# Optimization experiments

Measured on AMD Instinct MI355X. Metric: run time of the kernel, lower is better.

## Reference

```python
import jax, jax.numpy as jnp
import numpy as np

SIGMA_MIN, SIGMA_MAX = 0.03, 0.35
LAMBDA_GEO = 8.0
COMPAT_SCALE = 0.1
INVALID_W = 0.05
NH, HD = 8, 64
LN_EPS = 1e-5

def _ln(x, g, b):
    m = x.mean(-1, keepdims=True)
    v = ((x - m) ** 2).mean(-1, keepdims=True)
    return (x - m) * jax.lax.rsqrt(v + LN_EPS) * g + b

def setup_inputs() -> dict:
    key = jax.random.key(0)
    ks = jax.random.split(key, 32)
    B, C, H, W = 8, 512, 32, 32
    T, S, D, SIN = 1024, 1024, 512, 512
    s = 0.02
    inp = {
        'front_feat': jax.random.normal(ks[0], (B, C, H, W), jnp.float32),
        'sat_tokens': jax.random.normal(ks[1], (B, S, SIN), jnp.float32),
        'sat_xy': jax.random.uniform(ks[2], (B, S, 2), jnp.float32),
        'front_bev_xy': jax.random.uniform(ks[3], (B, T, 2), jnp.float32),
        'front_bev_valid_mask': jax.random.bernoulli(ks[4], 0.9, (B, T)),
        'front_plucker': jax.random.normal(ks[5], (B, T, 6), jnp.float32),
        'fa_w': jax.random.normal(ks[6], (C, D), jnp.float32) * s,
        'fa_b': jnp.zeros((D,), jnp.float32),
        'fa_g': jnp.ones((D,), jnp.float32),
        'fa_lb': jnp.zeros((D,), jnp.float32),
        'sa_w': jax.random.normal(ks[7], (SIN, D), jnp.float32) * s,
        'sa_b': jnp.zeros((D,), jnp.float32),
        'sa_g': jnp.ones((D,), jnp.float32),
        'sa_lb': jnp.zeros((D,), jnp.float32),
        'q_w': jax.random.normal(ks[8], (D, D), jnp.float32) * s,
        'q_b': jnp.zeros((D,), jnp.float32),
        'k_w': jax.random.normal(ks[9], (D, D), jnp.float32) * s,
        'k_b': jnp.zeros((D,), jnp.float32),
        'v_w': jax.random.normal(ks[10], (D, D), jnp.float32) * s,
        'v_b': jnp.zeros((D,), jnp.float32),
        'pl_w1': jax.random.normal(ks[11], (6, D), jnp.float32) * s,
        'pl_b1': jnp.zeros((D,), jnp.float32),
        'pl_w2': jax.random.normal(ks[12], (D, D), jnp.float32) * s,
        'pl_b2': jnp.zeros((D,), jnp.float32),
        'sig_w': jax.random.normal(ks[13], (D, 1), jnp.float32) * s,
        'sig_b': jnp.zeros((1,), jnp.float32),
        'db_w': jax.random.normal(ks[14], (D, NH), jnp.float32) * s,
        'db_b': jnp.zeros((NH,), jnp.float32),
        'out_w': jax.random.normal(ks[15], (D, C), jnp.float32) * s,
        'out_b': jnp.zeros((C,), jnp.float32),
    }
    return inp

def _forward(front_feat, sat_tokens, sat_xy, front_bev_xy, front_plucker,
             fa_w, fa_b, fa_g, fa_lb, sa_w, sa_b, sa_g, sa_lb,
             q_w, q_b, k_w, k_b, v_w, v_b, pl_w1, pl_b1, pl_w2, pl_b2,
             sig_w, sig_b, db_w, db_b, out_w, out_b, valid_mask):
    B, C, H, W = front_feat.shape
    T = H * W
    D = NH * HD
    front_flat = front_feat.reshape(B, C, T).transpose(0, 2, 1)  # [B,T,C]
    front_embed = _ln(front_flat @ fa_w + fa_b, fa_g, fa_lb)
    pl = jax.nn.silu(front_plucker @ pl_w1 + pl_b1) @ pl_w2 + pl_b2
    context = front_embed + pl
    sat_embed = _ln(sat_tokens @ sa_w + sa_b, sa_g, sa_lb)
    def heads(x):
        return x.reshape(B, -1, NH, HD).transpose(0, 2, 1, 3)  # [B,H,N,d]
    q = heads(front_embed @ q_w + q_b)
    k = heads(sat_embed @ k_w + k_b)
    v = heads(sat_embed @ v_w + v_b)
    compat = jnp.einsum('bhtd,bhsd->bhts', q, k) / jnp.sqrt(jnp.float32(HD))
    compat = COMPAT_SCALE * compat
    sigma = SIGMA_MIN + (SIGMA_MAX - SIGMA_MIN) * jax.nn.sigmoid((context @ sig_w + sig_b)[..., 0])  # [B,T]
    dist2 = ((front_bev_xy[:, :, None, :] - sat_xy[:, None, :, :]) ** 2).sum(-1)  # [B,T,S]
    geo = -LAMBDA_GEO * dist2 / jnp.maximum(sigma[..., None] ** 2, 1e-6)
    sat_logits = compat + geo[:, None]  # [B,H,T,S]
    sat_logits = jnp.where(valid_mask[:, None, :, None], sat_logits, jnp.float32(-10000.0))
    dustbin = (context @ db_w + db_b).transpose(0, 2, 1)[..., None]  # [B,H,T,1]
    logits = jnp.concatenate([sat_logits, dustbin], axis=-1)
    probs = jax.nn.softmax(logits, axis=-1)
    sat_probs, dustbin_prob = probs[..., :-1], probs[..., -1]
    read = jnp.einsum('bhts,bhsd->bhtd', sat_probs, v)
    read = read.transpose(0, 2, 1, 3).reshape(B, T, D)
    read_feat = (read @ out_w + out_b).transpose(0, 2, 1).reshape(B, C, H, W)
    confidence = (1.0 - dustbin_prob).mean(axis=1)  # [B,T]
    conf_feat = confidence.reshape(B, 1, H, W)
    front_feat_out = front_feat + conf_feat * read_feat
    vf = valid_mask.astype(confidence.dtype)
    inv = 1.0 - vf
    invalid_conf = (confidence * inv).sum() / jnp.maximum(inv.sum(), 1.0)
    invalid_conf_loss = invalid_conf * INVALID_W
    return front_feat_out, read_feat, confidence, invalid_conf_loss

def reference(front_feat, sat_tokens, sat_xy, front_bev_xy, front_bev_valid_mask, front_plucker,
              fa_w, fa_b, fa_g, fa_lb, sa_w, sa_b, sa_g, sa_lb,
              q_w, q_b, k_w, k_b, v_w, v_b, pl_w1, pl_b1, pl_w2, pl_b2,
              sig_w, sig_b, db_w, db_b, out_w, out_b):
    return _forward(front_feat, sat_tokens, sat_xy, front_bev_xy, front_plucker,
                    fa_w, fa_b, fa_g, fa_lb, sa_w, sa_b, sa_g, sa_lb,
                    q_w, q_b, k_w, k_b, v_w, v_b, pl_w1, pl_b1, pl_w2, pl_b2,
                    sig_w, sig_b, db_w, db_b, out_w, out_b, front_bev_valid_mask)
```

## Files before the change

kernel.cpp:

```cpp
#include <hip/hip_runtime.h>

typedef unsigned short u16;
typedef __attribute__((ext_vector_type(8))) short short8;
typedef __attribute__((ext_vector_type(4))) float f32x4;

constexpr int B_  = 8;
constexpr int C_  = 512;
constexpr int T_  = 1024;
constexpr int S_  = 1024;
constexpr int D_  = 512;
constexpr int NH_ = 8;
constexpr int BT_ = B_ * T_;
constexpr float INVLN2 = 1.44269504088896340736f;
constexpr float QSCALE2 = 0.0125f * INVLN2;

__device__ __forceinline__ unsigned pack2(float lo, float hi) {
    unsigned r;
    asm("v_cvt_pk_bf16_f32 %0, %1, %2" : "=v"(r) : "v"(lo), "v"(hi));
    return r;
}
__device__ __forceinline__ u16 f2bf(float x) {
    return (u16)pack2(x, x);
}
__device__ __forceinline__ float bf2f(u16 h) {
    union { unsigned u; float f; } v; v.u = ((unsigned)h) << 16;
    return v.f;
}
__device__ __forceinline__ float fexp2(float x) {
    float r;
    asm("v_exp_f32 %0, %1" : "=v"(r) : "v"(x));
    return r;
}
__device__ __forceinline__ float max3f(float a, float b, float c) {
    float r;
    asm("v_max3_f32 %0, %1, %2, %3" : "=v"(r) : "v"(a), "v"(b), "v"(c));
    return r;
}

#define GWAITBAR(N) do { \
    asm volatile("s_waitcnt vmcnt(" #N ") lgkmcnt(0)" ::: "memory"); \
    __builtin_amdgcn_sched_barrier(0); \
    __builtin_amdgcn_s_barrier(); \
    __builtin_amdgcn_sched_barrier(0); } while (0)

typedef __attribute__((address_space(3))) unsigned int lds_u32;
typedef const __attribute__((address_space(1))) unsigned int glob_u32;
__device__ __forceinline__ void g2l16(void* l, const void* g) {
    __builtin_amdgcn_global_load_lds((glob_u32*)g, (lds_u32*)l, 16, 0, 0);
}

__device__ __forceinline__ int is_valid(const void* mask, int mode, int idx) {
    if (mode == 0) return ((const int*)mask)[idx] != 0;
    if (mode == 1) return ((const float*)mask)[idx] != 0.0f;
    return ((const unsigned char*)mask)[idx] != 0;
}

__global__ __launch_bounds__(256) void prep_k(
    const float* __restrict__ ff, const float* __restrict__ sat,
    const float* __restrict__ pl,
    const float* a0, const float* a1, const float* a2, const float* a3,
    const float* a4, const float* a5, u16* __restrict__ WT,
    u16* __restrict__ ffb, u16* __restrict__ satb,
    const float* __restrict__ plw1, const float* __restrict__ plb1,
    u16* __restrict__ plh,
    const unsigned* __restrict__ maskw, int* __restrict__ mode,
    float* __restrict__ scal,
    const float* __restrict__ plw2, const float* __restrict__ sigw,
    const float* __restrict__ dbw, const float* __restrict__ plb2,
    float* __restrict__ wsig, float* __restrict__ wdbf,
    float* __restrict__ offs) {
    __shared__ float tile[32][33];
    int blk = blockIdx.x, tid = threadIdx.x;
    if (blk < 4096) {
        int t0 = (blk & 31) * 32, c0 = ((blk >> 5) & 15) * 32, b = blk >> 9;
        int tx = tid & 31, ty = tid >> 5;
        const float* ip = ff + (size_t)b * C_ * T_;
        for (int i = ty; i < 32; i += 8)
            tile[i][tx] = ip[(size_t)(c0 + i) * T_ + t0 + tx];
        __syncthreads();
        u16* op = ffb + (size_t)b * T_ * C_;
        for (int i = ty; i < 32; i += 8)
            op[(size_t)(t0 + i) * C_ + c0 + tx] = f2bf(tile[tx][i]);
    } else if (blk < 5632) {
        int idx = blk - 4096;
        const float* srcs[6] = {a0, a1, a2, a3, a4, a5};
        int z = idx >> 8;
        const float* src = srcs[z];
        u16* d = WT + (size_t)z * 512 * 512;
        int k0 = (idx & 15) * 32, n0 = ((idx >> 4) & 15) * 32;
        int tx = tid & 31, ty = tid >> 5;
        for (int i = ty; i < 32; i += 8)
            tile[i][tx] = src[(size_t)(k0 + i) * 512 + n0 + tx];
        __syncthreads();
        for (int i = ty; i < 32; i += 8)
            d[(size_t)(n0 + i) * 512 + k0 + tx] = f2bf(tile[tx][i]);
    } else if (blk < 7680) {
        int i = (blk - 5632) * 256 + tid;
        const float4* p = (const float4*)(sat + (size_t)i * 8);
        float4 a = p[0], b = p[1];
        uint4 o;
        o.x = pack2(a.x, a.y); o.y = pack2(a.z, a.w);
        o.z = pack2(b.x, b.y); o.w = pack2(b.z, b.w);
        *(uint4*)(satb + (size_t)i * 8) = o;
    } else if (blk < 9728) {
        int m = (blk - 7680) * 4 + (tid >> 6);
        int lane = tid & 63;
        float p6[6];
#pragma unroll
        for (int j = 0; j < 6; ++j) p6[j] = pl[(size_t)m * 6 + j];
        int n0 = lane * 8;
        float acc[8];
#pragma unroll
        for (int e = 0; e < 8; ++e) acc[e] = plb1[n0 + e];
#pragma unroll
        for (int j = 0; j < 6; ++j) {
            float4 wv0 = *(const float4*)(plw1 + j * D_ + n0);
            float4 wv1 = *(const float4*)(plw1 + j * D_ + n0 + 4);
            acc[0] += p6[j] * wv0.x; acc[1] += p6[j] * wv0.y;
            acc[2] += p6[j] * wv0.z; acc[3] += p6[j] * wv0.w;
            acc[4] += p6[j] * wv1.x; acc[5] += p6[j] * wv1.y;
            acc[6] += p6[j] * wv1.z; acc[7] += p6[j] * wv1.w;
        }
        uint4 o;
        float s0 = acc[0] / (1.0f + __expf(-acc[0]));
        float s1 = acc[1] / (1.0f + __expf(-acc[1]));
        float s2 = acc[2] / (1.0f + __expf(-acc[2]));
        float s3 = acc[3] / (1.0f + __expf(-acc[3]));
        float s4 = acc[4] / (1.0f + __expf(-acc[4]));
        float s5 = acc[5] / (1.0f + __expf(-acc[5]));
        float s6 = acc[6] / (1.0f + __expf(-acc[6]));
        float s7 = acc[7] / (1.0f + __expf(-acc[7]));
        o.x = pack2(s0, s1); o.y = pack2(s2, s3);
        o.z = pack2(s4, s5); o.w = pack2(s6, s7);
        *(uint4*)(plh + (size_t)m * D_ + n0) = o;
    } else if (blk == 9728) {
        __shared__ int bad_i, bad_f;
        if (tid == 0) { bad_i = 0; bad_f = 0; }
        __syncthreads();
        for (int i = tid; i < 2048; i += 256) {
            unsigned v = maskw[i];
            if (v > 1u) bad_i = 1;
            if (v != 0u && v != 0x3f800000u) bad_f = 1;
        }
        __syncthreads();
        if (tid == 0) {
            *mode = (!bad_i) ? 0 : ((!bad_f) ? 1 : 2);
            scal[0] = 0.0f; scal[1] = 0.0f;
        }
    } else if (blk < 9731) {
        int k = (blk - 9729) * 256 + tid;
        const float* wr = plw2 + (size_t)k * 512;
        float acc = 0;
        for (int n = 0; n < 512; n += 4) {
            float4 wv = *(const float4*)(wr + n);
            float4 sv = *(const float4*)(sigw + n);
            acc += wv.x * sv.x + wv.y * sv.y + wv.z * sv.z + wv.w * sv.w;
        }
        wsig[k] = acc;
    } else if (blk < 9747) {
        int idx = blk - 9731;
        int k = idx * 32 + (tid >> 3), h = tid & 7;
        const float* wr = plw2 + (size_t)k * 512;
        float acc = 0;
        for (int n = 0; n < 512; ++n) acc += wr[n] * dbw[n * 8 + h];
        wdbf[k * 8 + h] = acc;
    } else {
        float p = plb2[tid] * sigw[tid] + plb2[tid + 256] * sigw[tid + 256];
        float ph[8];
#pragma unroll
        for (int h = 0; h < 8; ++h)
            ph[h] = plb2[tid] * dbw[tid * 8 + h] +
                    plb2[tid + 256] * dbw[(tid + 256) * 8 + h];
        for (int o = 32; o; o >>= 1) {
            p += __shfl_down(p, o);
#pragma unroll
            for (int h = 0; h < 8; ++h) ph[h] += __shfl_down(ph[h], o);
        }
        __shared__ float red[4][9];
        int wv = tid >> 6, lane = tid & 63;
        if (lane == 0) {
            red[wv][0] = p;
#pragma unroll
            for (int h = 0; h < 8; ++h) red[wv][1 + h] = ph[h];
        }
        __syncthreads();
        if (tid == 0) {
            for (int j = 0; j < 9; ++j) {
                float t = 0;
                for (int v2 = 0; v2 < 4; ++v2) t += red[v2][j];
                offs[j] = t;
            }
        }
    }
}

__global__ __launch_bounds__(256) void gmm_k(
    const u16* __restrict__ A0, const u16* __restrict__ A1,
    const u16* __restrict__ A2, const u16* __restrict__ A3,
    const u16* __restrict__ Bt0, const u16* __restrict__ Bt1,
    const u16* __restrict__ Bt2, const u16* __restrict__ Bt3,
    const float* __restrict__ bb0, const float* __restrict__ bb1,
    const float* __restrict__ bb2, const float* __restrict__ bb3,
    void* __restrict__ C0v, void* __restrict__ C1v,
    void* __restrict__ C2v, void* __restrict__ C3v,
    int md0, int md1, int md2, int md3,
    const u16* __restrict__ addend,
    const float* __restrict__ ffp, float* __restrict__ out1p,
    const float* __restrict__ dbpp, const void* __restrict__ maskp,
    const int* __restrict__ modep, float* __restrict__ outcp,
    float* __restrict__ scalp) {
    __shared__ u16 As[3][4096];
    __shared__ u16 Bs[3][4096];
    __shared__ float confL[128];
    int jid = blockIdx.x >> 8;
    int L = blockIdx.x & 255;
    const u16* A    = (jid == 0) ? A0 : (jid == 1) ? A1 : (jid == 2) ? A2 : A3;
    const u16* Bt   = (jid == 0) ? Bt0 : (jid == 1) ? Bt1 : (jid == 2) ? Bt2 : Bt3;
    const float* bias = (jid == 0) ? bb0 : (jid == 1) ? bb1 : (jid == 2) ? bb2 : bb3;
    void* Cv        = (jid == 0) ? C0v : (jid == 1) ? C1v : (jid == 2) ? C2v : C3v;
    int mode        = (jid == 0) ? md0 : (jid == 1) ? md1 : (jid == 2) ? md2 : md3;

    int tid = threadIdx.x, w = tid >> 6, l = tid & 63;
    int lr = l & 15, g = l >> 4;
    int W = (L & 7) * 32 + (L >> 3);
    int m0 = (W >> 2) * 128, n0 = (W & 3) * 128;
    int wr = w >> 1, wc = w & 1;
    int prm = g ^ ((lr >> 1) & 3);

    f32x4 acc[4][4] = {};

    if (mode == 4 && tid < 128) {
        int row = m0 + tid;
        const float* dr = dbpp + (size_t)row * NH_;
        float s = 0;
#pragma unroll
        for (int h = 0; h < 8; ++h) s += dr[h];
        float cf = 1.0f - s * 0.125f;
        confL[tid] = cf;
        if ((W & 3) == 0) {
            outcp[row] = cf;
            int md = *modep;
            float invd = is_valid(maskp, md, row) ? 0.0f : 1.0f;
            float a = cf * invd, bsum = invd;
            for (int o = 32; o; o >>= 1) {
                a += __shfl_down(a, o);
                bsum += __shfl_down(bsum, o);
            }
            if ((tid & 63) == 0) {
                atomicAdd(&scalp[0], a);
                atomicAdd(&scalp[1], bsum);
            }
        }
    }

    auto stage = [&](int buf, int k0) {
#pragma unroll
        for (int j = 0; j < 2; ++j) {
            int i = tid + 256 * j;
            int row = i >> 2, gg = (i & 3) ^ ((i >> 3) & 3);
            g2l16((char*)As[buf] + (size_t)i * 16,
                  A + (size_t)(m0 + row) * 512 + k0 + gg * 8);
        }
#pragma unroll
        for (int j = 0; j < 2; ++j) {
            int i = tid + 256 * j;
            int col = i >> 2, gg = (i & 3) ^ ((i >> 3) & 3);
            g2l16((char*)Bs[buf] + (size_t)i * 16,
                  Bt + (size_t)(n0 + col) * 512 + k0 + gg * 8);
        }
    };

    auto compute = [&](int bi) {
        const char* Ab = (const char*)As[bi];
        const char* Bb = (const char*)Bs[bi];
        short8 af[4], bf[4];
#pragma unroll
        for (int m = 0; m < 4; ++m)
            af[m] = *(const short8*)(Ab + ((wr * 64 + m * 16 + lr) * 4 + prm) * 16);
#pragma unroll
        for (int n = 0; n < 4; ++n)
            bf[n] = *(const short8*)(Bb + ((wc * 64 + n * 16 + lr) * 4 + prm) * 16);
        __builtin_amdgcn_s_setprio(1);
#pragma unroll
        for (int m = 0; m < 4; ++m)
#pragma unroll
            for (int n = 0; n < 4; ++n)
                acc[m][n] = __builtin_amdgcn_mfma_f32_16x16x32_bf16(
                    af[m], bf[n], acc[m][n], 0, 0, 0);
        __builtin_amdgcn_s_setprio(0);
    };

    stage(0, 0);
    stage(1, 32);
    for (int t = 0; t < 14; ++t) {
        stage((t + 2) % 3, (t + 2) * 32);
        GWAITBAR(8);
        compute(t % 3);
        __builtin_amdgcn_s_barrier();
    }
    GWAITBAR(4);
    compute(2);
    GWAITBAR(0);
    compute(0);

    float bs[4];
#pragma unroll
    for (int n = 0; n < 4; ++n) bs[n] = bias[n0 + wc * 64 + n * 16 + lr];

#pragma unroll
    for (int m = 0; m < 4; ++m) {
#pragma unroll
        for (int n = 0; n < 4; ++n) {
            int R0  = m0 + wr * 64 + m * 16 + 4 * g;
            int col = n0 + wc * 64 + n * 16 + lr;
            if (mode == 3) {
                int bbx = R0 >> 10, ss = R0 & 1023, hh = col >> 6, dd = col & 63;
                uint2 pk;
                pk.x = pack2(acc[m][n][0] + bs[n], acc[m][n][1] + bs[n]);
                pk.y = pack2(acc[m][n][2] + bs[n], acc[m][n][3] + bs[n]);
                u16* dst = (u16*)Cv + ((size_t)(bbx * 8 + hh) * 64 + dd) * 1024 + ss;
                *(uint2*)dst = pk;
            } else if (mode == 4) {
                int bbx = R0 >> 10, t0p = R0 & 1023;
                size_t base = (size_t)bbx * C_ * T_ + (size_t)col * T_ + t0p;
                float4 rf;
                rf.x = acc[m][n][0] + bs[n]; rf.y = acc[m][n][1] + bs[n];
                rf.z = acc[m][n][2] + bs[n]; rf.w = acc[m][n][3] + bs[n];
                float4 ffv = *(const float4*)(ffp + base);
                float4 cfv = *(const float4*)&confL[R0 - m0];
                float4 o0v;
                o0v.x = ffv.x + cfv.x * rf.x; o0v.y = ffv.y + cfv.y * rf.y;
                o0v.z = ffv.z + cfv.z * rf.z; o0v.w = ffv.w + cfv.w * rf.w;
                *(float4*)(out1p + base) = rf;
                *(float4*)((float*)Cv + base) = o0v;
            } else {
#pragma unroll
                for (int j = 0; j < 4; ++j) {
                    int row = R0 + j;
                    float v = acc[m][n][j] + bs[n];
                    if (mode == 1) v *= QSCALE2;
                    if (mode == 2) v += bf2f(addend[(size_t)row * 512 + col]);
                    ((u16*)Cv)[(size_t)row * 512 + col] = f2bf(v);
                }
            }
        }
    }
}

__global__ __launch_bounds__(256) void lnh_k(
    const u16* __restrict__ Epre, const float* __restrict__ fg,
    const float* __restrict__ fb, u16* __restrict__ Eout,
    const u16* __restrict__ Spre, const float* __restrict__ sg,
    const float* __restrict__ sb, u16* __restrict__ Sout,
    const u16* __restrict__ PLH,
    const float* __restrict__ sigw, const float* __restrict__ sigb,
    const float* __restrict__ dbw, const float* __restrict__ dbb,
    const float* __restrict__ wsig, const float* __restrict__ wdbf,
    const float* __restrict__ offs,
    float* __restrict__ sigma, float* __restrict__ dbo) {
    int blk = blockIdx.x, tid = threadIdx.x;
    int wv = tid >> 6, lane = tid & 63;
    if (blk < 4096) {
        int sel = blk >> 11;
        int row = (blk & 2047) * 4 + wv;
        const u16* X = sel ? Spre : Epre;
        const float* gw = sel ? sg : fg;
        const float* bw = sel ? sb : fb;
        u16* out = sel ? Sout : Eout;
        uint4 u = *((const uint4*)(X + (size_t)row * 512) + lane);
        float x[8];
        x[0] = bf2f((u16)(u.x & 0xffff)); x[1] = bf2f((u16)(u.x >> 16));
        x[2] = bf2f((u16)(u.y & 0xffff)); x[3] = bf2f((u16)(u.y >> 16));
        x[4] = bf2f((u16)(u.z & 0xffff)); x[5] = bf2f((u16)(u.z >> 16));
        x[6] = bf2f((u16)(u.w & 0xffff)); x[7] = bf2f((u16)(u.w >> 16));
        float s = 0, sq = 0;
#pragma unroll
        for (int i = 0; i < 8; ++i) { s += x[i]; sq += x[i] * x[i]; }
        for (int o = 1; o < 64; o <<= 1) {
            s += __shfl_xor(s, o); sq += __shfl_xor(sq, o);
        }
        float mean = s * (1.0f / D_);
        float var  = sq * (1.0f / D_) - mean * mean;
        float r = rsqrtf(var + 1e-5f);
        float4 g0v = *(const float4*)(gw + lane * 8);
        float4 g1v = *(const float4*)(gw + lane * 8 + 4);
        float4 b0v = *(const float4*)(bw + lane * 8);
        float4 b1v = *(const float4*)(bw + lane * 8 + 4);
        float gv[8] = {g0v.x, g0v.y, g0v.z, g0v.w, g1v.x, g1v.y, g1v.z, g1v.w};
        float bv[8] = {b0v.x, b0v.y, b0v.z, b0v.w, b1v.x, b1v.y, b1v.z, b1v.w};
        uint4 o;
        float y[8];
#pragma unroll
        for (int i = 0; i < 8; ++i) y[i] = (x[i] - mean) * r * gv[i] + bv[i];
        o.x = pack2(y[0], y[1]); o.y = pack2(y[2], y[3]);
        o.z = pack2(y[4], y[5]); o.w = pack2(y[6], y[7]);
        *((uint4*)(out + (size_t)row * 512) + lane) = o;
    } else {
        int row = (blk - 4096) * 4 + wv;
        uint4 u = *((const uint4*)(Epre + (size_t)row * 512) + lane);
        float x[8];
        x[0] = bf2f((u16)(u.x & 0xffff)); x[1] = bf2f((u16)(u.x >> 16));
        x[2] = bf2f((u16)(u.y & 0xffff)); x[3] = bf2f((u16)(u.y >> 16));
        x[4] = bf2f((u16)(u.z & 0xffff)); x[5] = bf2f((u16)(u.z >> 16));
        x[6] = bf2f((u16)(u.w & 0xffff)); x[7] = bf2f((u16)(u.w >> 16));
        float s = 0, sq = 0;
#pragma unroll
        for (int i = 0; i < 8; ++i) { s += x[i]; sq += x[i] * x[i]; }
        for (int o = 1; o < 64; o <<= 1) {
            s += __shfl_xor(s, o); sq += __shfl_xor(sq, o);
        }
        float mean = s * (1.0f / D_);
        float var  = sq * (1.0f / D_) - mean * mean;
        float r = rsqrtf(var + 1e-5f);
        float4 g0v = *(const float4*)(fg + lane * 8);
        float4 g1v = *(const float4*)(fg + lane * 8 + 4);
        float4 b0v = *(const float4*)(fb + lane * 8);
        float4 b1v = *(const float4*)(fb + lane * 8 + 4);
        float gv[8] = {g0v.x, g0v.y, g0v.z, g0v.w, g1v.x, g1v.y, g1v.z, g1v.w};
        float bv[8] = {b0v.x, b0v.y, b0v.z, b0v.w, b1v.x, b1v.y, b1v.z, b1v.w};
        float E[8];
#pragma unroll
        for (int i = 0; i < 8; ++i) E[i] = (x[i] - mean) * r * gv[i] + bv[i];
        uint4 up = *((const uint4*)(PLH + (size_t)row * 512) + lane);
        float plv[8];
        plv[0] = bf2f((u16)(up.x & 0xffff)); plv[1] = bf2f((u16)(up.x >> 16));
        plv[2] = bf2f((u16)(up.y & 0xffff)); plv[3] = bf2f((u16)(up.y >> 16));
        plv[4] = bf2f((u16)(up.z & 0xffff)); plv[5] = bf2f((u16)(up.z >> 16));
        plv[6] = bf2f((u16)(up.w & 0xffff)); plv[7] = bf2f((u16)(up.w >> 16));
        float4 sw0 = *(const float4*)(sigw + lane * 8);
        float4 sw1 = *(const float4*)(sigw + lane * 8 + 4);
        float4 fw0 = *(const float4*)(wsig + lane * 8);
        float4 fw1 = *(const float4*)(wsig + lane * 8 + 4);
        float swv[8] = {sw0.x, sw0.y, sw0.z, sw0.w, sw1.x, sw1.y, sw1.z, sw1.w};
        float fwv[8] = {fw0.x, fw0.y, fw0.z, fw0.w, fw1.x, fw1.y, fw1.z, fw1.w};
        float sacc = 0;
#pragma unroll
        for (int i = 0; i < 8; ++i) sacc += E[i] * swv[i] + plv[i] * fwv[i];
        float d_[8] = {};
        const float* dr = dbw + (size_t)lane * 8 * NH_;
        const float* fr = wdbf + (size_t)lane * 8 * NH_;
#pragma unroll
        for (int i = 0; i < 8; ++i) {
#pragma unroll
            for (int h = 0; h < 8; ++h)
                d_[h] += E[i] * dr[i * NH_ + h] + plv[i] * fr[i * NH_ + h];
        }
        for (int o = 1; o < 64; o <<= 1) {
            sacc += __shfl_xor(sacc, o);
#pragma unroll
            for (int h = 0; h < 8; ++h) d_[h] += __shfl_xor(d_[h], o);
        }
        if (lane == 0) {
            float z = sacc + sigb[0] + offs[0];
            sigma[row] = 0.03f + 0.32f / (1.0f + __expf(-z));
            float* dd = dbo + (size_t)row * NH_;
#pragma unroll
            for (int h = 0; h < 8; ++h) dd[h] = d_[h] + dbb[h] + offs[1 + h];
        }
    }
}

__global__ __launch_bounds__(512) void attn_k(
    const u16* __restrict__ Q, const u16* __restrict__ K,
    const u16* __restrict__ Vt, const float* __restrict__ sig,
    const float* __restrict__ dbl, const float* __restrict__ bev,
    const float* __restrict__ sxy, const void* __restrict__ mask,
    const int* __restrict__ mode, u16* __restrict__ OUT,
    float* __restrict__ dbp) {
    int L = blockIdx.x;
    int W = (L & 7) * 64 + (L >> 3);
    int b = W >> 6, h = (W >> 3) & 7, tblk = W & 7;
    int tid = threadIdx.x, w = tid >> 6, l = tid & 63;
    int lr = l & 15, g = l >> 4;
    int p8 = lr & 7;

    __shared__ u16 Kbuf[2][4096];
    __shared__ u16 Vbuf[2][4096];
    __shared__ float2 SXY[1024];
    __shared__ float  SZ[1024];

    const float2* xp = (const float2*)(sxy + (size_t)b * S_ * 2);
#pragma unroll
    for (int j = 0; j < 2; ++j) {
        int idx = tid + 512 * j;
        float2 v = xp[idx];
        SXY[idx] = make_float2(-2.0f * v.x, -2.0f * v.y);
        SZ[idx] = v.x * v.x + v.y * v.y;
    }

    int trow = b * T_ + tblk * 128 + w * 16 + lr;
    float s_ = sig[trow];
    float bx = bev[(size_t)trow * 2], by = bev[(size_t)trow * 2 + 1];
    float dbv2 = dbl[(size_t)trow * NH_ + h] * INVLN2;
    int md = *mode;
    bool vld = is_valid(mask, md, trow) != 0;
    float grow  = vld ? (-11.5415603271117f / fmaxf(s_ * s_, 1e-6f)) : 0.0f;
    float Abase = vld ? grow * (bx * bx + by * by) : -10000.0f;
    float AbaseM = Abase - dbv2;
    float mshift = 0.0f;

    const u16* qp = Q + (size_t)trow * 512 + h * 64 + g * 8;
    short8 q0 = *(const short8*)qp;
    short8 q1 = *(const short8*)(qp + 32);
    if (!vld) { q0 = short8{}; q1 = short8{}; }

    short8 ones;
#pragma unroll
    for (int e = 0; e < 8; ++e) ones[e] = (short)0x3F80;

    const u16* Kp = K + (size_t)b * S_ * 512 + h * 64;
    const u16* Vp = Vt + (size_t)(b * 8 + h) * 64 * 1024;

    int srow = tid >> 3;
    int gprm = (tid & 7) ^ (srow & 7);
    int sK = ((srow >> 5) & 1) * 32 + ((srow >> 2) & 3) * 8 +
             ((srow >> 4) & 1) * 4 + (srow & 3);

    auto stageKV = [&](int buf, int s0) {
        g2l16((char*)Kbuf[buf] + (size_t)tid * 16,
              Kp + (size_t)(s0 + sK) * 512 + gprm * 8);
        g2l16((char*)Vbuf[buf] + (size_t)tid * 16,
              Vp + (size_t)srow * 1024 + s0 + gprm * 8);
    };

    f32x4 o0 = {}, o1 = {}, o2 = {}, o3 = {};
    f32x4 o4 = {1.0f, 1.0f, 1.0f, 1.0f};

    stageKV(0, 0);
    int cur = 0;
    for (int c = 0; c < 16; ++c) {
        int s0c = c * 64;
        if (c < 15) {
            stageKV(cur ^ 1, s0c + 64);
            GWAITBAR(2);
        } else {
            GWAITBAR(0);
        }

        const char* Kc = (const char*)Kbuf[cur];
        const char* Vc = (const char*)Vbuf[cur];

        f32x4 p[4];
        f32x4 z4 = {};
        __builtin_amdgcn_s_setprio(1);
#pragma unroll
        for (int sub = 0; sub < 4; ++sub) {
            int krow = sub * 16 + lr;
            short8 kf0 = *(const short8*)(Kc + (krow * 8 + (g ^ p8)) * 16);
            short8 kf1 = *(const short8*)(Kc + (krow * 8 + ((4 + g) ^ p8)) * 16);
            p[sub] = __builtin_amdgcn_mfma_f32_16x16x32_bf16(kf0, q0, z4, 0, 0, 0);
            p[sub] = __builtin_amdgcn_mfma_f32_16x16x32_bf16(kf1, q1, p[sub], 0, 0, 0);
        }
        __builtin_amdgcn_s_setprio(0);

        float lg[16];
#pragma unroll
        for (int sub = 0; sub < 4; ++sub) {
            int sl = s0c + ((sub & 2) << 4) + 8 * g + ((sub & 1) << 2);
            float4 xy01 = *(const float4*)&SXY[sl];
            float4 xy23 = *(const float4*)&SXY[sl + 2];
            float4 zz   = *(const float4*)&SZ[sl];
            float X[4] = {xy01.x, xy01.z, xy23.x, xy23.z};
            float Y[4] = {xy01.y, xy01.w, xy23.y, xy23.w};
            float Z[4] = {zz.x, zz.y, zz.z, zz.w};
#pragma unroll
            for (int i2 = 0; i2 < 4; ++i2) {
                float wg = fmaf(bx, X[i2], fmaf(by, Y[i2], Z[i2]));
                lg[sub * 4 + i2] = fmaf(grow, wg, p[sub][i2] + AbaseM);
            }
        }
        float c0 = max3f(lg[0], lg[1], lg[2]);
        float c1 = max3f(lg[3], lg[4], lg[5]);
        float c2 = max3f(lg[6], lg[7], lg[8]);
        float c3 = max3f(lg[9], lg[10], lg[11]);
        float c4 = max3f(lg[12], lg[13], lg[14]);
        float cl = fmaxf(max3f(c0, c1, c2), max3f(c3, c4, lg[15]));

        if (!__all(cl <= 11.5f)) {
            cl = fmaxf(cl, __shfl_xor(cl, 16));
            cl = fmaxf(cl, __shfl_xor(cl, 32));
            float dm = fmaxf(cl, 0.0f);
            float scl = fexp2(-dm);
            o0 *= scl; o1 *= scl; o2 *= scl; o3 *= scl; o4 *= scl;
            AbaseM -= dm;
            mshift -= dm;
#pragma unroll
            for (int r = 0; r < 16; ++r) lg[r] -= dm;
        }
        float pe[16];
#pragma unroll
        for (int r = 0; r < 16; ++r) pe[r] = fexp2(lg[r]);

        union { uint4 u; short8 s8; } pf0, pf1;
        pf0.u.x = pack2(pe[0], pe[1]);  pf0.u.y = pack2(pe[2], pe[3]);
        pf0.u.z = pack2(pe[4], pe[5]);  pf0.u.w = pack2(pe[6], pe[7]);
        pf1.u.x = pack2(pe[8], pe[9]);  pf1.u.y = pack2(pe[10], pe[11]);
        pf1.u.z = pack2(pe[12], pe[13]); pf1.u.w = pack2(pe[14], pe[15]);

        __builtin_amdgcn_s_setprio(1);
        short8 vf;
#pragma unroll
        for (int dt = 0; dt < 4; ++dt) {
            int vrow = dt * 16 + lr;
            f32x4* oo = (dt == 0) ? &o0 : (dt == 1) ? &o1 : (dt == 2) ? &o2 : &o3;
            vf = *(const short8*)(Vc + (vrow * 8 + (g ^ p8)) * 16);
            *oo = __builtin_amdgcn_mfma_f32_16x16x32_bf16(vf, pf0.s8, *oo, 0, 0, 0);
            vf = *(const short8*)(Vc + (vrow * 8 + ((4 + g) ^ p8)) * 16);
            *oo = __builtin_amdgcn_mfma_f32_16x16x32_bf16(vf, pf1.s8, *oo, 0, 0, 0);
        }
        o4 = __builtin_amdgcn_mfma_f32_16x16x32_bf16(ones, pf0.s8, o4, 0, 0, 0);
        o4 = __builtin_amdgcn_mfma_f32_16x16x32_bf16(ones, pf1.s8, o4, 0, 0, 0);
        __builtin_amdgcn_s_setprio(0);

        __builtin_amdgcn_s_barrier();
        cur ^= 1;
    }

    float inv = 1.0f / o4[0];
    u16* ob = OUT + (size_t)trow * 512 + h * 64;
    {
        uint2 pk;
        pk.x = pack2(o0[0] * inv, o0[1] * inv); pk.y = pack2(o0[2] * inv, o0[3] * inv);
        *(uint2*)(ob + 0 * 16 + 4 * g) = pk;
        pk.x = pack2(o1[0] * inv, o1[1] * inv); pk.y = pack2(o1[2] * inv, o1[3] * inv);
        *(uint2*)(ob + 1 * 16 + 4 * g) = pk;
        pk.x = pack2(o2[0] * inv, o2[1] * inv); pk.y = pack2(o2[2] * inv, o2[3] * inv);
        *(uint2*)(ob + 2 * 16 + 4 * g) = pk;
        pk.x = pack2(o3[0] * inv, o3[1] * inv); pk.y = pack2(o3[2] * inv, o3[3] * inv);
        *(uint2*)(ob + 3 * 16 + 4 * g) = pk;
    }
    if (g == 0) dbp[(size_t)trow * NH_ + h] = fexp2(mshift) * inv;
}

__global__ void loss_k(const float* __restrict__ scal, float* __restrict__ out) {
    out[0] = scal[0] / fmaxf(scal[1], 1.0f) * 0.05f;
}

extern "C" void kernel_launch(void* const* d_in, const int* in_sizes, int n_in,
                              void* d_out, int out_size, void* d_ws, size_t ws_size,
                              hipStream_t stream) {
    const float* front_feat = (const float*)d_in[0];
    const float* sat_tokens = (const float*)d_in[1];
    const float* sat_xy     = (const float*)d_in[2];
    const float* bev_xy     = (const float*)d_in[3];
    const void*  mask       = d_in[4];
    const float* plucker    = (const float*)d_in[5];
    const float* fa_w = (const float*)d_in[6];
    const float* fa_b = (const float*)d_in[7];
    const float* fa_g = (const float*)d_in[8];
    const float* fa_lb = (const float*)d_in[9];
    const float* sa_w = (const float*)d_in[10];
    const float* sa_b = (const float*)d_in[11];
    const float* sa_g = (const float*)d_in[12];
    const float* sa_lb = (const float*)d_in[13];
    const float* q_w = (const float*)d_in[14];
    const float* q_b = (const float*)d_in[15];
    const float* k_w = (const float*)d_in[16];
    const float* k_b = (const float*)d_in[17];
    const float* v_w = (const float*)d_in[18];
    const float* v_b = (const float*)d_in[19];
    const float* pl_w1 = (const float*)d_in[20];
    const float* pl_b1 = (const float*)d_in[21];
    const float* pl_w2 = (const float*)d_in[22];
    const float* pl_b2 = (const float*)d_in[23];
    const float* sig_w = (const float*)d_in[24];
    const float* sig_b = (const float*)d_in[25];
    const float* db_w = (const float*)d_in[26];
    const float* db_b = (const float*)d_in[27];
    const float* out_w = (const float*)d_in[28];
    const float* out_b = (const float*)d_in[29];

    char* w8 = (char*)d_ws;
    u16* H0 = (u16*)(w8);
    u16* H1 = (u16*)(w8 + 8388608ull * 1);
    u16* H2 = (u16*)(w8 + 8388608ull * 2);
    u16* H3 = (u16*)(w8 + 8388608ull * 3);
    u16* H4 = (u16*)(w8 + 8388608ull * 4);
    u16* H5 = (u16*)(w8 + 8388608ull * 5);
    u16* H6 = (u16*)(w8 + 8388608ull * 6);
    u16* WT = (u16*)(w8 + 8388608ull * 7);
    char* sm = w8 + 8388608ull * 7 + 3670016ull;
    float* w_sigma = (float*)sm;
    float* w_db    = w_sigma + BT_;
    float* w_dbp   = w_db + (size_t)BT_ * NH_;
    float* w_scal  = w_dbp + (size_t)BT_ * NH_;
    int*   w_mode  = (int*)(w_scal + 2);
    float* w_wsig  = w_scal + 4;
    float* w_wdbf  = w_wsig + 512;
    float* w_offs  = w_wdbf + 4096;

    u16* Wfa = WT;                 u16* Wq  = WT + 262144ull * 1;
    u16* Wsa = WT + 262144ull * 2; u16* Wk  = WT + 262144ull * 3;
    u16* Wv  = WT + 262144ull * 4; u16* Wo  = WT + 262144ull * 5;

    float* out0 = (float*)d_out;
    float* out1 = out0 + (size_t)B_ * C_ * T_;
    float* outc = out1 + (size_t)B_ * C_ * T_;
    float* outl = outc + (size_t)B_ * T_;

    dim3 blk(256);

    prep_k<<<dim3(9748), blk, 0, stream>>>(
        front_feat, sat_tokens, plucker,
        fa_w, q_w, sa_w, k_w, v_w, out_w, WT,
        H0, H5, pl_w1, pl_b1, H2,
        (const unsigned*)mask, w_mode, w_scal,
        pl_w2, sig_w, db_w, pl_b2, w_wsig, w_wdbf, w_offs);
    gmm_k<<<dim3(512), blk, 0, stream>>>(
        H0, H5, nullptr, nullptr,
        Wfa, Wsa, nullptr, nullptr,
        fa_b, sa_b, nullptr, nullptr,
        H6, H4, nullptr, nullptr,
        0, 0, 0, 0,
        nullptr, nullptr, nullptr,
        nullptr, nullptr, nullptr, nullptr, nullptr);
    lnh_k<<<dim3(6144), blk, 0, stream>>>(
        H6, fa_g, fa_lb, H1,
        H4, sa_g, sa_lb, H3,
        H2, sig_w, sig_b, db_w, db_b,
        w_wsig, w_wdbf, w_offs, w_sigma, w_db);
    gmm_k<<<dim3(768), blk, 0, stream>>>(
        H1, H3, H3, nullptr,
        Wq, Wk, Wv, nullptr,
        q_b, k_b, v_b, nullptr,
        H5, H0, H4, nullptr,
        1, 0, 3, 0,
        nullptr, nullptr, nullptr,
        nullptr, nullptr, nullptr, nullptr, nullptr);
    attn_k<<<dim3(512), dim3(512), 0, stream>>>(
        H5, H0, H4, w_sigma, w_db, bev_xy, sat_xy, mask, w_mode, H2, w_dbp);
    gmm_k<<<dim3(256), blk, 0, stream>>>(
        H2, nullptr, nullptr, nullptr,
        Wo, nullptr, nullptr, nullptr,
        out_b, nullptr, nullptr, nullptr,
        out0, nullptr, nullptr, nullptr,
        4, 0, 0, 0,
        nullptr, front_feat, out1,
        w_dbp, mask, w_mode, outc, w_scal);
    loss_k<<<1, 1, 0, stream>>>(w_scal, outl);
}
```

Measured before the change: 170.3 us.

## Split LayerNorm and head projection kernels, transpose dustbin weights for vector loads

```diff
diff --git a/kernel.cpp b/kernel.cpp
--- a/kernel.cpp
+++ b/kernel.cpp
@@ -67,8 +67,8 @@
     float* __restrict__ scal,
     const float* __restrict__ plw2, const float* __restrict__ sigw,
     const float* __restrict__ dbw, const float* __restrict__ plb2,
-    float* __restrict__ wsig, float* __restrict__ wdbf,
-    float* __restrict__ offs) {
+    float* __restrict__ wsig, float* __restrict__ wdbfT,
+    float* __restrict__ offs, float* __restrict__ dbwT) {
     __shared__ float tile[32][33];
     int blk = blockIdx.x, tid = threadIdx.x;
     if (blk < 4096) {
@@ -163,8 +163,8 @@
         const float* wr = plw2 + (size_t)k * 512;
         float acc = 0;
         for (int n = 0; n < 512; ++n) acc += wr[n] * dbw[n * 8 + h];
-        wdbf[k * 8 + h] = acc;
-    } else {
+        wdbfT[h * 512 + k] = acc;
+    } else if (blk == 9747) {
         float p = plb2[tid] * sigw[tid] + plb2[tid + 256] * sigw[tid + 256];
         float ph[8];
 #pragma unroll
@@ -190,6 +190,11 @@
                 for (int v2 = 0; v2 < 4; ++v2) t += red[v2][j];
                 offs[j] = t;
             }
+        }
+    } else {
+        for (int i = tid; i < 4096; i += 256) {
+            int h = i >> 9, n = i & 511;
+            dbwT[h * 512 + n] = dbw[n * 8 + h];
         }
     }
 }
@@ -347,116 +352,101 @@
     }
 }
 
-__global__ __launch_bounds__(256) void lnh_k(
-    const u16* __restrict__ Epre, const float* __restrict__ fg,
-    const float* __restrict__ fb, u16* __restrict__ Eout,
-    const u16* __restrict__ Spre, const float* __restrict__ sg,
-    const float* __restrict__ sb, u16* __restrict__ Sout,
-    const u16* __restrict__ PLH,
+__global__ __launch_bounds__(256) void ln2_k(
+    const u16* __restrict__ X0, const float* __restrict__ g0,
+    const float* __restrict__ b0, u16* __restrict__ O0,
+    const u16* __restrict__ X1, const float* __restrict__ g1,
+    const float* __restrict__ b1, u16* __restrict__ O1) {
+    int sel = blockIdx.x >> 13;
+    int row = blockIdx.x & 8191;
+    const u16* X = sel ? X1 : X0;
+    const float* gw = sel ? g1 : g0;
+    const float* bw = sel ? b1 : b0;
+    u16* out = sel ? O1 : O0;
+    int tid = threadIdx.x;
+    const unsigned* xr = (const unsigned*)(X + (size_t)row * D_);
+    unsigned u = xr[tid];
+    float x0 = bf2f((u16)(u & 0xffff)), x1 = bf2f((u16)(u >> 16));
+    float s = x0 + x1, sq = x0 * x0 + x1 * x1;
+    __shared__ float rs[4], rq[4];
+    for (int o = 32; o; o >>= 1) { s += __shfl_down(s, o); sq += __shfl_down(sq, o); }
+    int wid = tid >> 6, lane = tid & 63;
+    if (lane == 0) { rs[wid] = s; rq[wid] = sq; }
+    __syncthreads();
+    if (tid == 0) {
+        float ts = 0, tq = 0;
+        for (int w = 0; w < 4; ++w) { ts += rs[w]; tq += rq[w]; }
+        rs[0] = ts; rq[0] = tq;
+    }
+    __syncthreads();
+    float mean = rs[0] * (1.0f / D_);
+    float var  = rq[0] * (1.0f / D_) - mean * mean;
+    float r = rsqrtf(var + 1e-5f);
+    float2 g2 = *(const float2*)(gw + 2 * tid);
+    float2 b2 = *(const float2*)(bw + 2 * tid);
+    float y0 = (x0 - mean) * r * g2.x + b2.x;
+    float y1 = (x1 - mean) * r * g2.y + b2.y;
+    ((unsigned*)(out + (size_t)row * D_))[tid] = pack2(y0, y1);
+}
+
+__global__ __launch_bounds__(256) void head2_k(
+    const u16* __restrict__ E, const u16* __restrict__ PLH,
     const float* __restrict__ sigw, const float* __restrict__ sigb,
-    const float* __restrict__ dbw, const float* __restrict__ dbb,
-    const float* __restrict__ wsig, const float* __restrict__ wdbf,
+    const float* __restrict__ wsig, const float* __restrict__ dbwT,
+    const float* __restrict__ wdbfT, const float* __restrict__ dbb,
     const float* __restrict__ offs,
     float* __restrict__ sigma, float* __restrict__ dbo) {
-    int blk = blockIdx.x, tid = threadIdx.x;
-    int wv = tid >> 6, lane = tid & 63;
-    if (blk < 4096) {
-        int sel = blk >> 11;
-        int row = (blk & 2047) * 4 + wv;
-        const u16* X = sel ? Spre : Epre;
-        const float* gw = sel ? sg : fg;
-        const float* bw = sel ? sb : fb;
-        u16* out = sel ? Sout : Eout;
-        uint4 u = *((const uint4*)(X + (size_t)row * 512) + lane);
-        float x[8];
-        x[0] = bf2f((u16)(u.x & 0xffff)); x[1] = bf2f((u16)(u.x >> 16));
-        x[2] = bf2f((u16)(u.y & 0xffff)); x[3] = bf2f((u16)(u.y >> 16));
-        x[4] = bf2f((u16)(u.z & 0xffff)); x[5] = bf2f((u16)(u.z >> 16));
-        x[6] = bf2f((u16)(u.w & 0xffff)); x[7] = bf2f((u16)(u.w >> 16));
-        float s = 0, sq = 0;
-#pragma unroll
-        for (int i = 0; i < 8; ++i) { s += x[i]; sq += x[i] * x[i]; }
-        for (int o = 1; o < 64; o <<= 1) {
-            s += __shfl_xor(s, o); sq += __shfl_xor(sq, o);
-        }
-        float mean = s * (1.0f / D_);
-        float var  = sq * (1.0f / D_) - mean * mean;
-        float r = rsqrtf(var + 1e-5f);
-        float4 g0v = *(const float4*)(gw + lane * 8);
-        float4 g1v = *(const float4*)(gw + lane * 8 + 4);
-        float4 b0v = *(const float4*)(bw + lane * 8);
-        float4 b1v = *(const float4*)(bw + lane * 8 + 4);
-        float gv[8] = {g0v.x, g0v.y, g0v.z, g0v.w, g1v.x, g1v.y, g1v.z, g1v.w};
-        float bv[8] = {b0v.x, b0v.y, b0v.z, b0v.w, b1v.x, b1v.y, b1v.z, b1v.w};
-        uint4 o;
-        float y[8];
-#pragma unroll
-        for (int i = 0; i < 8; ++i) y[i] = (x[i] - mean) * r * gv[i] + bv[i];
-        o.x = pack2(y[0], y[1]); o.y = pack2(y[2], y[3]);
-        o.z = pack2(y[4], y[5]); o.w = pack2(y[6], y[7]);
-        *((uint4*)(out + (size_t)row * 512) + lane) = o;
-    } else {
-        int row = (blk - 4096) * 4 + wv;
-        uint4 u = *((const uint4*)(Epre + (size_t)row * 512) + lane);
-        float x[8];
-        x[0] = bf2f((u16)(u.x & 0xffff)); x[1] = bf2f((u16)(u.x >> 16));
-        x[2] = bf2f((u16)(u.y & 0xffff)); x[3] = bf2f((u16)(u.y >> 16));
-        x[4] = bf2f((u16)(u.z & 0xffff)); x[5] = bf2f((u16)(u.z >> 16));
-        x[6] = bf2f((u16)(u.w & 0xffff)); x[7] = bf2f((u16)(u.w >> 16));
-        float s = 0, sq = 0;
-#pragma unroll
-        for (int i = 0; i < 8; ++i) { s += x[i]; sq += x[i] * x[i]; }
-        for (int o = 1; o < 64; o <<= 1) {
-            s += __shfl_xor(s, o); sq += __shfl_xor(sq, o);
-        }
-        float mean = s * (1.0f / D_);
-        float var  = sq * (1.0f / D_) - mean * mean;
-        float r = rsqrtf(var + 1e-5f);
-        float4 g0v = *(const float4*)(fg + lane * 8);
-        float4 g1v = *(const float4*)(fg + lane * 8 + 4);
-        float4 b0v = *(const float4*)(fb + lane * 8);
-        float4 b1v = *(const float4*)(fb + lane * 8 + 4);
-        float gv[8] = {g0v.x, g0v.y, g0v.z, g0v.w, g1v.x, g1v.y, g1v.z, g1v.w};
-        float bv[8] = {b0v.x, b0v.y, b0v.z, b0v.w, b1v.x, b1v.y, b1v.z, b1v.w};
-        float E[8];
-#pragma unroll
-        for (int i = 0; i < 8; ++i) E[i] = (x[i] - mean) * r * gv[i] + bv[i];
-        uint4 up = *((const uint4*)(PLH + (size_t)row * 512) + lane);
-        float plv[8];
-        plv[0] = bf2f((u16)(up.x & 0xffff)); plv[1] = bf2f((u16)(up.x >> 16));
-        plv[2] = bf2f((u16)(up.y & 0xffff)); plv[3] = bf2f((u16)(up.y >> 16));
-        plv[4] = bf2f((u16)(up.z & 0xffff)); plv[5] = bf2f((u16)(up.z >> 16));
-        plv[6] = bf2f((u16)(up.w & 0xffff)); plv[7] = bf2f((u16)(up.w >> 16));
-        float4 sw0 = *(const float4*)(sigw + lane * 8);
-        float4 sw1 = *(const float4*)(sigw + lane * 8 + 4);
-        float4 fw0 = *(const float4*)(wsig + lane * 8);
-        float4 fw1 = *(const float4*)(wsig + lane * 8 + 4);
-        float swv[8] = {sw0.x, sw0.y, sw0.z, sw0.w, sw1.x, sw1.y, sw1.z, sw1.w};
-        float fwv[8] = {fw0.x, fw0.y, fw0.z, fw0.w, fw1.x, fw1.y, fw1.z, fw1.w};
-        float sacc = 0;
-#pragma unroll
-        for (int i = 0; i < 8; ++i) sacc += E[i] * swv[i] + plv[i] * fwv[i];
-        float d_[8] = {};
-        const float* dr = dbw + (size_t)lane * 8 * NH_;
-        const float* fr = wdbf + (size_t)lane * 8 * NH_;
-#pragma unroll
-        for (int i = 0; i < 8; ++i) {
-#pragma unroll
-            for (int h = 0; h < 8; ++h)
-                d_[h] += E[i] * dr[i * NH_ + h] + plv[i] * fr[i * NH_ + h];
-        }
-        for (int o = 1; o < 64; o <<= 1) {
-            sacc += __shfl_xor(sacc, o);
-#pragma unroll
-            for (int h = 0; h < 8; ++h) d_[h] += __shfl_xor(d_[h], o);
-        }
-        if (lane == 0) {
-            float z = sacc + sigb[0] + offs[0];
-            sigma[row] = 0.03f + 0.32f / (1.0f + __expf(-z));
-            float* dd = dbo + (size_t)row * NH_;
-#pragma unroll
-            for (int h = 0; h < 8; ++h) dd[h] = d_[h] + dbb[h] + offs[1 + h];
-        }
+    int wv = threadIdx.x >> 6, lane = threadIdx.x & 63;
+    int row = blockIdx.x * 4 + wv;
+    uint4 ue = *((const uint4*)(E + (size_t)row * 512) + lane);
+    float Ev[8];
+    Ev[0] = bf2f((u16)(ue.x & 0xffff)); Ev[1] = bf2f((u16)(ue.x >> 16));
+    Ev[2] = bf2f((u16)(ue.y & 0xffff)); Ev[3] = bf2f((u16)(ue.y >> 16));
+    Ev[4] = bf2f((u16)(ue.z & 0xffff)); Ev[5] = bf2f((u16)(ue.z >> 16));
+    Ev[6] = bf2f((u16)(ue.w & 0xffff)); Ev[7] = bf2f((u16)(ue.w >> 16));
+    uint4 up = *((const uint4*)(PLH + (size_t)row * 512) + lane);
+    float plv[8];
+    plv[0] = bf2f((u16)(up.x & 0xffff)); plv[1] = bf2f((u16)(up.x >> 16));
+    plv[2] = bf2f((u16)(up.y & 0xffff)); plv[3] = bf2f((u16)(up.y >> 16));
+    plv[4] = bf2f((u16)(up.z & 0xffff)); plv[5] = bf2f((u16)(up.z >> 16));
+    plv[6] = bf2f((u16)(up.w & 0xffff)); plv[7] = bf2f((u16)(up.w >> 16));
+
+    int n0 = lane * 8;
+    float4 sw0 = *(const float4*)(sigw + n0);
+    float4 sw1 = *(const float4*)(sigw + n0 + 4);
+    float4 fw0 = *(const float4*)(wsig + n0);
+    float4 fw1 = *(const float4*)(wsig + n0 + 4);
+    float swv[8] = {sw0.x, sw0.y, sw0.z, sw0.w, sw1.x, sw1.y, sw1.z, sw1.w};
+    float fwv[8] = {fw0.x, fw0.y, fw0.z, fw0.w, fw1.x, fw1.y, fw1.z, fw1.w};
+    float sacc = 0;
+#pragma unroll
+    for (int i = 0; i < 8; ++i) sacc += Ev[i] * swv[i] + plv[i] * fwv[i];
+
+    float d_[8];
+#pragma unroll
+    for (int h = 0; h < 8; ++h) {
+        const float* ar = dbwT + h * 512 + n0;
+        const float* br = wdbfT + h * 512 + n0;
+        float4 a0v = *(const float4*)ar;
+        float4 a1v = *(const float4*)(ar + 4);
+        float4 b0v = *(const float4*)br;
+        float4 b1v = *(const float4*)(br + 4);
+        d_[h] = Ev[0] * a0v.x + Ev[1] * a0v.y + Ev[2] * a0v.z + Ev[3] * a0v.w +
+                Ev[4] * a1v.x + Ev[5] * a1v.y + Ev[6] * a1v.z + Ev[7] * a1v.w +
+                plv[0] * b0v.x + plv[1] * b0v.y + plv[2] * b0v.z + plv[3] * b0v.w +
+                plv[4] * b1v.x + plv[5] * b1v.y + plv[6] * b1v.z + plv[7] * b1v.w;
+    }
+    for (int o = 1; o < 64; o <<= 1) {
+        sacc += __shfl_xor(sacc, o);
+#pragma unroll
+        for (int h = 0; h < 8; ++h) d_[h] += __shfl_xor(d_[h], o);
+    }
+    if (lane == 0) {
+        float z = sacc + sigb[0] + offs[0];
+        sigma[row] = 0.03f + 0.32f / (1.0f + __expf(-z));
+        float* dd = dbo + (size_t)row * NH_;
+#pragma unroll
+        for (int h = 0; h < 8; ++h) dd[h] = d_[h] + dbb[h] + offs[1 + h];
     }
 }
 
@@ -686,8 +676,9 @@
     float* w_scal  = w_dbp + (size_t)BT_ * NH_;
     int*   w_mode  = (int*)(w_scal + 2);
     float* w_wsig  = w_scal + 4;
-    float* w_wdbf  = w_wsig + 512;
-    float* w_offs  = w_wdbf + 4096;
+    float* w_wdbfT = w_wsig + 512;
+    float* w_offs  = w_wdbfT + 4096;
+    float* w_dbwT  = w_offs + 16;
 
     u16* Wfa = WT;                 u16* Wq  = WT + 262144ull * 1;
     u16* Wsa = WT + 262144ull * 2; u16* Wk  = WT + 262144ull * 3;
@@ -700,12 +691,12 @@
 
     dim3 blk(256);
 
-    prep_k<<<dim3(9748), blk, 0, stream>>>(
+    prep_k<<<dim3(9749), blk, 0, stream>>>(
         front_feat, sat_tokens, plucker,
         fa_w, q_w, sa_w, k_w, v_w, out_w, WT,
         H0, H5, pl_w1, pl_b1, H2,
         (const unsigned*)mask, w_mode, w_scal,
-        pl_w2, sig_w, db_w, pl_b2, w_wsig, w_wdbf, w_offs);
+        pl_w2, sig_w, db_w, pl_b2, w_wsig, w_wdbfT, w_offs, w_dbwT);
     gmm_k<<<dim3(512), blk, 0, stream>>>(
         H0, H5, nullptr, nullptr,
         Wfa, Wsa, nullptr, nullptr,
@@ -714,11 +705,11 @@
         0, 0, 0, 0,
         nullptr, nullptr, nullptr,
         nullptr, nullptr, nullptr, nullptr, nullptr);
-    lnh_k<<<dim3(6144), blk, 0, stream>>>(
-        H6, fa_g, fa_lb, H1,
-        H4, sa_g, sa_lb, H3,
-        H2, sig_w, sig_b, db_w, db_b,
-        w_wsig, w_wdbf, w_offs, w_sigma, w_db);
+    ln2_k<<<dim3(16384), blk, 0, stream>>>(H6, fa_g, fa_lb, H1,
+                                           H4, sa_g, sa_lb, H3);
+    head2_k<<<dim3(2048), blk, 0, stream>>>(
+        H1, H2, sig_w, sig_b, w_wsig, w_dbwT, w_wdbfT, db_b, w_offs,
+        w_sigma, w_db);
     gmm_k<<<dim3(768), blk, 0, stream>>>(
         H1, H3, H3, nullptr,
         Wq, Wk, Wv, nullptr,
```

Result: faster. 156.6 us (-8.0%).
